# Kernel tuning notes

Measured on AMD Instinct MI355X. Metric: run time of the kernel, lower is better.

The kernel has to match this reference:

```python
import jax, jax.numpy as jnp
import numpy as np

N = 8192
D = 512
H = 256
K_TOPK = 21  # k + 1 with k = 20
EPS_NORM = 1e-12
EPS_DEG = 1e-10


def setup_inputs() -> dict:
    key = jax.random.key(0)
    ks = jax.random.split(key, 10)
    s = 0.02  # small init scale so similarities are well-behaved
    return {
        "features": jax.random.normal(ks[0], (N, D), jnp.float32),
        "masked_features": jax.random.normal(ks[1], (N, D), jnp.float32),
        "W1": jax.random.normal(ks[2], (D, D), jnp.float32) * s,
        "b1": jax.random.normal(ks[3], (D,), jnp.float32) * s,
        "W2": jax.random.normal(ks[4], (D, D), jnp.float32) * s,
        "b2": jax.random.normal(ks[5], (D,), jnp.float32) * s,
        "Wg1": jax.random.normal(ks[6], (D, H), jnp.float32) * s,
        "bg1": jax.random.normal(ks[7], (H,), jnp.float32) * s,
        "Wg2": jax.random.normal(ks[8], (H, D), jnp.float32) * s,
        "bg2": jax.random.normal(ks[9], (D,), jnp.float32) * s,
    }


def reference(features, masked_features, W1, b1, W2, b2, Wg1, bg1, Wg2, bg2):
    # ---- graph generator MLP ----
    h = jax.nn.relu(features @ W1 + b1)            # [N, D]
    emb = h @ W2 + b2                              # [N, D]
    norm = jnp.linalg.norm(emb, axis=1, keepdims=True)
    emb = emb / jnp.maximum(norm, EPS_NORM)        # F.normalize(dim=1, p=2)
    sim = emb @ emb.T                              # [N, N] cosine similarity

    # ---- top-k mask (k+1 neighbors), zero diagonal ----
    _, idx = jax.lax.top_k(sim, K_TOPK)            # [N, K]
    rows = jnp.arange(N)[:, None]
    mask = jnp.zeros((N, N), sim.dtype).at[rows, idx].set(1.0)
    mask = mask * (1.0 - jnp.eye(N, dtype=sim.dtype))  # fill_diagonal_(0)
    mask = jax.lax.stop_gradient(mask)
    sim = jax.nn.relu(sim * mask)

    # ---- symmetrize ----
    gen_adj = (sim + sim.T) * 0.5                  # [N, N]

    # ---- degree norm: D^{-1/2} (A + I) D^{-1/2} ----
    A = gen_adj + jnp.eye(N, dtype=gen_adj.dtype)
    inv_sqrt_deg = 1.0 / (jnp.sqrt(A.sum(axis=1)) + EPS_DEG)
    A = inv_sqrt_deg[:, None] * A * inv_sqrt_deg[None, :]

    # ---- two dense GCN hops (dropout inert in eval mode) ----
    h1 = jax.nn.relu(A @ (masked_features @ Wg1 + bg1))  # [N, H]
    h3 = A @ (h1 @ Wg2 + bg2)                            # [N, D]
    return h3, gen_adj
```

## Files before the change

### kernel.cpp

```cpp
#include <hip/hip_runtime.h>
#include <cstdint>
#include <cstddef>

#define NN 8192
#define DD 512
#define HH 256
#define KTOP 21
#define CCAP 192
#define CMIN 48
#define ECAP 224
#define NBIN 1024

typedef __attribute__((ext_vector_type(8))) __bf16 bf16x8;
typedef __attribute__((ext_vector_type(4))) float f32x4;

__device__ __forceinline__ unsigned short f2bf(float x) {
    unsigned u = __float_as_uint(x);
    u += 0x7fffu + ((u >> 16) & 1u);
    return (unsigned short)(u >> 16);
}
__device__ __forceinline__ float bf2f(unsigned short h) {
    return __uint_as_float(((unsigned)h) << 16);
}
__device__ __forceinline__ unsigned ordkey(float x) {
    unsigned b = __float_as_uint(x);
    return b ^ (((int)b >> 31) | 0x80000000u);
}

#define GLD16(gp, lp) __builtin_amdgcn_global_load_lds( \
    (const __attribute__((address_space(1))) unsigned int*)(gp), \
    (__attribute__((address_space(3))) unsigned int*)(lp), 16, 0, 0)

template<bool TRANSB, int ACT>
__global__ __launch_bounds__(256)
void sgemm128(const float* __restrict__ A, const float* __restrict__ B,
              const float* __restrict__ bias, float* __restrict__ C,
              int M, int N, int K) {
    constexpr int BM = 128, BN = 128, BK = 16;
    __shared__ float As[BK][BM + 4];
    __shared__ float Bs[BK][BN + 4];

    const int tiles_n = N / BN;
    const int by = blockIdx.x / tiles_n;
    const int bx = blockIdx.x % tiles_n;
    const int row0 = by * BM, col0 = bx * BN;
    const int tid = threadIdx.x;
    const int tx = tid & 15, ty = tid >> 4;

    float acc[8][8];
#pragma unroll
    for (int m = 0; m < 8; ++m)
#pragma unroll
        for (int n = 0; n < 8; ++n) acc[m][n] = 0.f;

    for (int k0 = 0; k0 < K; k0 += BK) {
#pragma unroll
        for (int l = 0; l < 2; ++l) {
            int f = tid + l * 256;
            int r = f >> 2, c4 = f & 3;
            float4 v = *reinterpret_cast<const float4*>(
                A + (size_t)(row0 + r) * K + k0 + c4 * 4);
            As[c4 * 4 + 0][r] = v.x;
            As[c4 * 4 + 1][r] = v.y;
            As[c4 * 4 + 2][r] = v.z;
            As[c4 * 4 + 3][r] = v.w;
        }
        if (TRANSB) {
#pragma unroll
            for (int l = 0; l < 2; ++l) {
                int f = tid + l * 256;
                int r = f >> 2, c4 = f & 3;
                float4 v = *reinterpret_cast<const float4*>(
                    B + (size_t)(col0 + r) * K + k0 + c4 * 4);
                Bs[c4 * 4 + 0][r] = v.x;
                Bs[c4 * 4 + 1][r] = v.y;
                Bs[c4 * 4 + 2][r] = v.z;
                Bs[c4 * 4 + 3][r] = v.w;
            }
        } else {
#pragma unroll
            for (int l = 0; l < 2; ++l) {
                int f = tid + l * 256;
                int kr = f >> 5, n4 = f & 31;
                *reinterpret_cast<float4*>(&Bs[kr][n4 * 4]) =
                    *reinterpret_cast<const float4*>(
                        B + (size_t)(k0 + kr) * N + col0 + n4 * 4);
            }
        }
        __syncthreads();

#pragma unroll
        for (int kk = 0; kk < BK; ++kk) {
            float a[8], b[8];
            *(float4*)&a[0] = *(const float4*)&As[kk][ty * 8];
            *(float4*)&a[4] = *(const float4*)&As[kk][ty * 8 + 4];
            *(float4*)&b[0] = *(const float4*)&Bs[kk][tx * 8];
            *(float4*)&b[4] = *(const float4*)&Bs[kk][tx * 8 + 4];
#pragma unroll
            for (int m = 0; m < 8; ++m)
#pragma unroll
                for (int n = 0; n < 8; ++n)
                    acc[m][n] = fmaf(a[m], b[n], acc[m][n]);
        }
        __syncthreads();
    }

    const int crow = row0 + ty * 8;
    const int ccol = col0 + tx * 8;
    float bv[8];
#pragma unroll
    for (int n = 0; n < 8; ++n) bv[n] = bias ? bias[ccol + n] : 0.f;
#pragma unroll
    for (int m = 0; m < 8; ++m) {
        float o[8];
#pragma unroll
        for (int n = 0; n < 8; ++n) {
            float t = acc[m][n] + bv[n];
            if (ACT == 1) t = fmaxf(t, 0.f);
            o[n] = t;
        }
        *reinterpret_cast<float4*>(C + (size_t)(crow + m) * N + ccol)     = *(float4*)&o[0];
        *reinterpret_cast<float4*>(C + (size_t)(crow + m) * N + ccol + 4) = *(float4*)&o[4];
    }
}

__global__ __launch_bounds__(256)
void rownorm_kernel(float* __restrict__ emb) {
    const int row = blockIdx.x, tid = threadIdx.x;
    float* rp = emb + (size_t)row * DD;
    float v0 = rp[tid], v1 = rp[tid + 256];
    float sum = v0 * v0 + v1 * v1;
#pragma unroll
    for (int off = 32; off > 0; off >>= 1) sum += __shfl_down(sum, off, 64);
    __shared__ float ws[4];
    __shared__ float sc_sh;
    if ((tid & 63) == 0) ws[tid >> 6] = sum;
    __syncthreads();
    if (tid == 0) {
        float n = sqrtf(ws[0] + ws[1] + ws[2] + ws[3]);
        sc_sh = 1.0f / fmaxf(n, 1e-12f);
    }
    __syncthreads();
    float sc = sc_sh;
    rp[tid] = v0 * sc;
    rp[tid + 256] = v1 * sc;
}

__global__ __launch_bounds__(256)
void cast_bf16_kernel(const float* __restrict__ e, unsigned short* __restrict__ hi) {
    const int i = (blockIdx.x * 256 + threadIdx.x) * 4;
    float4 v = *reinterpret_cast<const float4*>(e + i);
    ushort4 h;
    h.x = f2bf(v.x); h.y = f2bf(v.y); h.z = f2bf(v.z); h.w = f2bf(v.w);
    *reinterpret_cast<ushort4*>(hi + i) = h;
}

__global__ __launch_bounds__(256)
void simgemm_bf16(const unsigned short* __restrict__ Ehi,
                  unsigned short* __restrict__ Cb) {
    const int bid = blockIdx.x;
    const int swz = (bid & 7) * 512 + (bid >> 3);
    const int by = swz >> 6, bx = swz & 63;

    __shared__ unsigned short Ah[128 * 32];
    __shared__ unsigned short Bh[128 * 32];

    const int tid = threadIdx.x, lane = tid & 63, wid = tid >> 6;
    const int wm = wid >> 1, wn = wid & 1;
    const int fr = lane & 15, fq = lane >> 4;
    const int lrow = lane >> 2;
    const int lcol8 = (lane & 3) * 8;

    const size_t arow0 = (size_t)by * 128;
    const size_t brow0 = (size_t)bx * 128;

    f32x4 acc[4][4];
#pragma unroll
    for (int m = 0; m < 4; ++m)
#pragma unroll
        for (int n = 0; n < 4; ++n) acc[m][n] = (f32x4){0.f, 0.f, 0.f, 0.f};

    for (int k0 = 0; k0 < DD; k0 += 32) {
#pragma unroll
        for (int i = 0; i < 2; ++i) {
            const int chunk = wid + i * 4;
            const int grow = chunk * 16 + lrow;
            GLD16(Ehi + (arow0 + grow) * DD + (k0 + lcol8), Ah + chunk * 512);
            GLD16(Ehi + (brow0 + grow) * DD + (k0 + lcol8), Bh + chunk * 512);
        }
        __syncthreads();

        bf16x8 ah[4], bh[4];
#pragma unroll
        for (int mf = 0; mf < 4; ++mf)
            ah[mf] = *(const bf16x8*)&Ah[(wm * 64 + mf * 16 + fr) * 32 + fq * 8];
#pragma unroll
        for (int nf = 0; nf < 4; ++nf)
            bh[nf] = *(const bf16x8*)&Bh[(wn * 64 + nf * 16 + fr) * 32 + fq * 8];
#pragma unroll
        for (int mf = 0; mf < 4; ++mf)
#pragma unroll
            for (int nf = 0; nf < 4; ++nf)
                acc[mf][nf] = __builtin_amdgcn_mfma_f32_16x16x32_bf16(ah[mf], bh[nf], acc[mf][nf], 0, 0, 0);
        __syncthreads();
    }

#pragma unroll
    for (int mf = 0; mf < 4; ++mf) {
#pragma unroll
        for (int nf = 0; nf < 4; ++nf) {
            const size_t row = arow0 + wm * 64 + mf * 16 + fq * 4;
            const int col = bx * 128 + wn * 64 + nf * 16 + fr;
#pragma unroll
            for (int r2 = 0; r2 < 4; ++r2)
                Cb[(row + r2) * NN + col] = f2bf(acc[mf][nf][r2]);
        }
    }
}

__global__ __launch_bounds__(256)
void topk_cand_kernel(const unsigned short* __restrict__ simb,
                      int* __restrict__ cand, int* __restrict__ ccnt) {
    const int row = blockIdx.x;
    const int tid = threadIdx.x;
    const int lane = tid & 63, wave = tid >> 6;
    const uint4* rp = reinterpret_cast<const uint4*>(simb + (size_t)row * NN);

    uint4 q[4];
#pragma unroll
    for (int t = 0; t < 4; ++t) q[t] = rp[t * 256 + tid];
    unsigned pk[16];
#pragma unroll
    for (int t = 0; t < 4; ++t) {
        pk[t * 4 + 0] = q[t].x; pk[t * 4 + 1] = q[t].y;
        pk[t * 4 + 2] = q[t].z; pk[t * 4 + 3] = q[t].w;
    }

    __shared__ int hist[NBIN];
    for (int b = tid; b < NBIN; b += 256) hist[b] = 0;
    __syncthreads();

    short bins[32];
#pragma unroll
    for (int u = 0; u < 16; ++u) {
        float flo = __uint_as_float(pk[u] << 16);
        float fhi = __uint_as_float(pk[u] & 0xFFFF0000u);
        int blo = (int)(flo * (float)NBIN); blo = max(0, min(NBIN - 1, blo));
        int bhi = (int)(fhi * (float)NBIN); bhi = max(0, min(NBIN - 1, bhi));
        bins[u * 2]     = (short)blo;
        bins[u * 2 + 1] = (short)bhi;
        atomicAdd(&hist[blo], 1);
        atomicAdd(&hist[bhi], 1);
    }
    __syncthreads();

    __shared__ int s_bstar;
    if (wave == 0) {
        int cum = 0, found = -1;
        for (int c0 = NBIN - 1; c0 >= 0 && found < 0; c0 -= 64) {
            int b = c0 - lane;
            int cnt = (b >= 0) ? hist[b] : 0;
            int sc = cnt;
#pragma unroll
            for (int off = 1; off < 64; off <<= 1) {
                int o = __shfl_up(sc, off, 64);
                if (lane >= off) sc += o;
            }
            int chunk_total = __shfl(sc, 63, 64);
            bool hit = (cum + sc >= CMIN);
            unsigned long long mh = __ballot(hit);
            if (mh) found = c0 - (__ffsll((long long)mh) - 1);
            else cum += chunk_total;
        }
        if (found < 0) found = 0;
        if (lane == 0) s_bstar = found;
    }
    __syncthreads();
    const int bstar = s_bstar;

    int cnt = 0;
#pragma unroll
    for (int i = 0; i < 32; ++i) cnt += (bins[i] >= bstar) ? 1 : 0;
    int sc = cnt;
#pragma unroll
    for (int off = 1; off < 64; off <<= 1) {
        int o = __shfl_up(sc, off, 64);
        if (lane >= off) sc += o;
    }
    __shared__ int wtot[4];
    if (lane == 63) wtot[wave] = sc;
    __syncthreads();
    int base = sc - cnt;
#pragma unroll
    for (int w = 0; w < 4; ++w)
        if (w < wave) base += wtot[w];
    int total = wtot[0] + wtot[1] + wtot[2] + wtot[3];

    int pos = base;
#pragma unroll
    for (int u = 0; u < 16; ++u) {
#pragma unroll
        for (int h = 0; h < 2; ++h) {
            if (bins[u * 2 + h] >= bstar) {
                if (pos < CCAP) {
                    int col = ((u >> 2) * 256 + tid) * 8 + (u & 3) * 2 + h;
                    cand[(size_t)row * CCAP + pos] = col;
                }
                pos++;
            }
        }
    }
    if (tid == 0) ccnt[row] = min(total, CCAP);
}

__global__ __launch_bounds__(256)
void refine_kernel(const float* __restrict__ emb, const int* __restrict__ cand,
                   const int* __restrict__ ccnt,
                   int* __restrict__ tidx, float* __restrict__ tval) {
    const int row = blockIdx.x;
    const int tid = threadIdx.x, lane = tid & 63, wv = tid >> 6;
    const int cnt = ccnt[row];
    __shared__ float sval[CCAP];
    __shared__ int   sidx[CCAP];
    const float* ei = emb + (size_t)row * DD;

    float4 a0 = reinterpret_cast<const float4*>(ei)[lane * 2];
    float4 a1 = reinterpret_cast<const float4*>(ei)[lane * 2 + 1];

    for (int base = wv * 2; base < cnt; base += 8) {
#pragma unroll
        for (int q = 0; q < 2; ++q) {
            int c = base + q;
            if (c >= cnt) break;
            const int j = cand[(size_t)row * CCAP + c];
            const float* ej = emb + (size_t)j * DD;
            float4 b0 = reinterpret_cast<const float4*>(ej)[lane * 2];
            float4 b1 = reinterpret_cast<const float4*>(ej)[lane * 2 + 1];
            float s = 0.f;
            s = fmaf(a0.x, b0.x, s); s = fmaf(a0.y, b0.y, s);
            s = fmaf(a0.z, b0.z, s); s = fmaf(a0.w, b0.w, s);
            s = fmaf(a1.x, b1.x, s); s = fmaf(a1.y, b1.y, s);
            s = fmaf(a1.z, b1.z, s); s = fmaf(a1.w, b1.w, s);
#pragma unroll
            for (int off = 32; off > 0; off >>= 1) s += __shfl_xor(s, off, 64);
            if (lane == 0) { sval[c] = s; sidx[c] = j; }
        }
    }
    __syncthreads();

    if (wv == 0) {
        float v[3]; int id[3];
#pragma unroll
        for (int k = 0; k < 3; ++k) {
            int s = lane + 64 * k;
            if (s < cnt) { v[k] = sval[s]; id[k] = sidx[s]; }
            else         { v[k] = -INFINITY; id[k] = 0x7fffffff; }
        }
#pragma unroll 1
        for (int sel = 0; sel < KTOP; ++sel) {
            float bv = v[0]; int bi = id[0];
#pragma unroll
            for (int k = 1; k < 3; ++k)
                if (v[k] > bv || (v[k] == bv && id[k] < bi)) { bv = v[k]; bi = id[k]; }
#pragma unroll
            for (int off = 1; off < 64; off <<= 1) {
                float ov = __shfl_xor(bv, off, 64);
                int   oi = __shfl_xor(bi, off, 64);
                if (ov > bv || (ov == bv && oi < bi)) { bv = ov; bi = oi; }
            }
            if (lane == 0) {
                tval[(size_t)row * KTOP + sel] = bv;
                tidx[(size_t)row * KTOP + sel] = bi;
            }
#pragma unroll
            for (int k = 0; k < 3; ++k)
                if (id[k] == bi) { v[k] = -INFINITY; id[k] = 0x7fffffff; }
        }
    }
}

__global__ __launch_bounds__(256)
void scatter_kernel(const int* __restrict__ tidx, const float* __restrict__ tval,
                    float* __restrict__ adj, int* __restrict__ ecnt,
                    int* __restrict__ ej, float* __restrict__ ev) {
    int t = blockIdx.x * 256 + threadIdx.x;
    if (t >= NN * KTOP) return;
    int i = t / KTOP;
    int j = tidx[t];
    if (j == i || j < 0) return;
    float v = tval[t];
    if (v <= 0.f) return;
    v *= 0.5f;
    atomicAdd(adj + (size_t)i * NN + j, v);
    atomicAdd(adj + (size_t)j * NN + i, v);
    int pi = atomicAdd(ecnt + i, 1);
    if (pi < ECAP) { ej[(size_t)i * ECAP + pi] = j; ev[(size_t)i * ECAP + pi] = v; }
    int pj = atomicAdd(ecnt + j, 1);
    if (pj < ECAP) { ej[(size_t)j * ECAP + pj] = i; ev[(size_t)j * ECAP + pj] = v; }
}

__global__ __launch_bounds__(256)
void sortdeg_kernel(int* __restrict__ ej, float* __restrict__ ev,
                    const int* __restrict__ ecnt, const float* __restrict__ adj,
                    float* __restrict__ sdeg) {
    const int row = blockIdx.x, tid = threadIdx.x;
    const int lane = tid & 63, wave = tid >> 6;
    const int nraw = ecnt[row];
    __shared__ float ws[4];

    if (nraw > ECAP) {
        const float4* rp = reinterpret_cast<const float4*>(adj + (size_t)row * NN);
        float sum = 0.f;
        for (int f = tid; f < NN / 4; f += 256) {
            float4 v = rp[f];
            sum += (v.x + v.y) + (v.z + v.w);
        }
#pragma unroll
        for (int off = 32; off > 0; off >>= 1) sum += __shfl_down(sum, off, 64);
        if (lane == 0) ws[wave] = sum;
        __syncthreads();
        if (tid == 0)
            sdeg[row] = 1.0f / (sqrtf(1.0f + ws[0] + ws[1] + ws[2] + ws[3]) + 1e-10f);
        return;
    }

    const int n = nraw;
    __shared__ int   lj[ECAP];
    __shared__ float lv[ECAP];
    __shared__ unsigned long long skey[ECAP];
    __shared__ int   oj[ECAP];
    __shared__ float ov[ECAP];
    if (tid < n) {
        int  jv = ej[(size_t)row * ECAP + tid];
        float vv = ev[(size_t)row * ECAP + tid];
        lj[tid] = jv; lv[tid] = vv;
        skey[tid] = ((unsigned long long)(unsigned)jv << 32) | (unsigned long long)ordkey(vv);
    }
    __syncthreads();
    if (tid < n) {
        unsigned long long mk = skey[tid];
        int rank = 0;
        for (int u = 0; u < n; ++u) {
            unsigned long long ku = skey[u];
            rank += (ku < mk || (ku == mk && u < tid)) ? 1 : 0;
        }
        oj[rank] = lj[tid];
        ov[rank] = lv[tid];
    }
    __syncthreads();
    if (tid < n) {
        ej[(size_t)row * ECAP + tid] = oj[tid];
        ev[(size_t)row * ECAP + tid] = ov[tid];
    }
    if (tid == 0) {
        float deg = 1.0f;
        for (int e = 0; e < n; ++e) deg += ov[e];
        sdeg[row] = 1.0f / (sqrtf(deg) + 1e-10f);
    }
}

template<int COLS, bool DORELU>
__global__ __launch_bounds__(256)
void spmm_edges(const int* __restrict__ ej, const float* __restrict__ ev,
                const int* __restrict__ ecnt, const float* __restrict__ adj,
                const float* __restrict__ sdeg,
                const float* __restrict__ X, float* __restrict__ Y) {
    constexpr int CPT = COLS / 256;
    const int i = blockIdx.x;
    const int tid = threadIdx.x;
    const int lane = tid & 63, wave = tid >> 6;
    const float si = sdeg[i];
    const int nraw = ecnt[i];

    float acc[CPT];
#pragma unroll
    for (int c = 0; c < CPT; ++c) acc[c] = 0.f;

    if (nraw <= ECAP) {
        __shared__ int   s_j[ECAP];
        __shared__ float s_w[ECAP];
        if (tid < nraw) {
            int j = ej[(size_t)i * ECAP + tid];
            s_j[tid] = j;
            s_w[tid] = ev[(size_t)i * ECAP + tid] * sdeg[j];
        }
        __syncthreads();
#pragma unroll 4
        for (int e = 0; e < nraw; ++e) {
            int j = s_j[e];
            float we = s_w[e];
#pragma unroll
            for (int c = 0; c < CPT; ++c)
                acc[c] += we * X[(size_t)j * COLS + tid + c * 256];
        }
    } else {
        __shared__ int   s_j[256];
        __shared__ float s_w[256];
        __shared__ int   s_cnt[4];
        const float* rowp = adj + (size_t)i * NN;
        for (int j0 = 0; j0 < NN; j0 += 256) {
            float w = rowp[j0 + tid];
            bool nz = (w != 0.f);
            unsigned long long m = __ballot(nz);
            unsigned long long ltmask = (lane == 0) ? 0ull : (~0ull >> (64 - lane));
            int pre = __popcll(m & ltmask);
            if (lane == 0) s_cnt[wave] = __popcll(m);
            __syncthreads();
            int base = 0;
#pragma unroll
            for (int q = 0; q < 4; ++q)
                if (q < wave) base += s_cnt[q];
            int total = s_cnt[0] + s_cnt[1] + s_cnt[2] + s_cnt[3];
            if (nz) {
                int p = base + pre;
                s_j[p] = j0 + tid;
                s_w[p] = w * sdeg[j0 + tid];
            }
            __syncthreads();
            for (int e = 0; e < total; ++e) {
                int j = s_j[e];
                float we = s_w[e];
#pragma unroll
                for (int c = 0; c < CPT; ++c)
                    acc[c] += we * X[(size_t)j * COLS + tid + c * 256];
            }
            __syncthreads();
        }
    }

#pragma unroll
    for (int c = 0; c < CPT; ++c) {
        float val = si * (acc[c] + si * X[(size_t)i * COLS + tid + c * 256]);
        if (DORELU) val = fmaxf(val, 0.f);
        Y[(size_t)i * COLS + tid + c * 256] = val;
    }
}

extern "C" void kernel_launch(void* const* d_in, const int* in_sizes, int n_in,
                              void* d_out, int out_size, void* d_ws, size_t ws_size,
                              hipStream_t stream) {
    const float* features = (const float*)d_in[0];
    const float* masked   = (const float*)d_in[1];
    const float* W1  = (const float*)d_in[2];
    const float* b1  = (const float*)d_in[3];
    const float* W2  = (const float*)d_in[4];
    const float* b2  = (const float*)d_in[5];
    const float* Wg1 = (const float*)d_in[6];
    const float* bg1 = (const float*)d_in[7];
    const float* Wg2 = (const float*)d_in[8];
    const float* bg2 = (const float*)d_in[9];

    float* out_h3  = (float*)d_out;
    float* out_adj = (float*)d_out + (size_t)NN * DD;
    unsigned short* simb = (unsigned short*)out_adj;

    float* h    = (float*)d_ws;
    unsigned short* hi = (unsigned short*)h;
    float* emb  = h + (size_t)NN * DD;
    float* tail = emb + (size_t)NN * DD;
    float* tval = tail;
    int*   tidx = (int*)(tval + (size_t)NN * KTOP);
    float* sdeg = (float*)(tidx + (size_t)NN * KTOP);
    int*   ecnt = (int*)(sdeg + NN);
    int*   ccnt = ecnt + NN;
    int*   elj  = ccnt + NN;
    float* elv  = (float*)(elj + (size_t)NN * ECAP);
    int*   cand = (int*)h;
    float* x1 = emb;
    float* h1 = emb + (size_t)NN * HH;
    float* x2 = h;

    dim3 blk(256);

    sgemm128<false, 1><<<dim3((NN / 128) * (DD / 128)), blk, 0, stream>>>(
        features, W1, b1, h, NN, DD, DD);
    sgemm128<false, 0><<<dim3((NN / 128) * (DD / 128)), blk, 0, stream>>>(
        h, W2, b2, emb, NN, DD, DD);
    rownorm_kernel<<<dim3(NN), blk, 0, stream>>>(emb);
    cast_bf16_kernel<<<dim3(NN * DD / 1024), blk, 0, stream>>>(emb, hi);
    simgemm_bf16<<<dim3(4096), blk, 0, stream>>>(hi, simb);
    topk_cand_kernel<<<dim3(NN), blk, 0, stream>>>(simb, cand, ccnt);
    refine_kernel<<<dim3(NN), blk, 0, stream>>>(emb, cand, ccnt, tidx, tval);
    hipMemsetAsync(out_adj, 0, (size_t)NN * NN * sizeof(float), stream);
    hipMemsetAsync(ecnt, 0, (size_t)NN * sizeof(int), stream);
    scatter_kernel<<<dim3((NN * KTOP + 255) / 256), blk, 0, stream>>>(
        tidx, tval, out_adj, ecnt, elj, elv);
    sortdeg_kernel<<<dim3(NN), blk, 0, stream>>>(elj, elv, ecnt, out_adj, sdeg);
    sgemm128<false, 0><<<dim3((NN / 128) * (HH / 128)), blk, 0, stream>>>(
        masked, Wg1, bg1, x1, NN, HH, DD);
    spmm_edges<HH, true><<<dim3(NN), blk, 0, stream>>>(
        elj, elv, ecnt, out_adj, sdeg, x1, h1);
    sgemm128<false, 0><<<dim3((NN / 128) * (DD / 128)), blk, 0, stream>>>(
        h1, Wg2, bg2, x2, NN, DD, HH);
    spmm_edges<DD, false><<<dim3(NN), blk, 0, stream>>>(
        elj, elv, ecnt, out_adj, sdeg, x2, out_h3);
}
```

Before: 802.1 us.

## Use split-bf16 MFMA for GCN GEMMs, fuse rownorm cast, custom zero kernel

The two GCN projection GEMMs move from the fp32 SIMT sgemm to a bf16x3 split-precision MFMA kernel (hi*hi + hi*lo + lo*hi). This needs extra split and weight-transpose kernels. The bf16 cast of the normalized embeddings is folded into the row-normalization kernel, which removes one pass over the embedding. The two memsets are replaced by a single grid-stride zero kernel. The aim is to trade fp32 FMA throughput for matrix-core throughput at slightly lower precision, at the cost of several extra small launches and workspace traffic.

After: 754.8 us. 5.9% less time.

```diff
diff --git a/kernel.cpp b/kernel.cpp
--- a/kernel.cpp
+++ b/kernel.cpp
@@ -125,7 +125,7 @@
 }
 
 __global__ __launch_bounds__(256)
-void rownorm_kernel(float* __restrict__ emb) {
+void rownorm_emit_kernel(float* __restrict__ emb, unsigned short* __restrict__ ehi) {
     const int row = blockIdx.x, tid = threadIdx.x;
     float* rp = emb + (size_t)row * DD;
     float v0 = rp[tid], v1 = rp[tid + 256];
@@ -142,17 +142,47 @@
     }
     __syncthreads();
     float sc = sc_sh;
-    rp[tid] = v0 * sc;
-    rp[tid + 256] = v1 * sc;
-}
-
-__global__ __launch_bounds__(256)
-void cast_bf16_kernel(const float* __restrict__ e, unsigned short* __restrict__ hi) {
+    v0 *= sc; v1 *= sc;
+    rp[tid] = v0;
+    rp[tid + 256] = v1;
+    ehi[(size_t)row * DD + tid]       = f2bf(v0);
+    ehi[(size_t)row * DD + tid + 256] = f2bf(v1);
+}
+
+__global__ __launch_bounds__(256)
+void split_kernel(const float* __restrict__ e, unsigned short* __restrict__ hi,
+                  unsigned short* __restrict__ lo) {
     const int i = (blockIdx.x * 256 + threadIdx.x) * 4;
     float4 v = *reinterpret_cast<const float4*>(e + i);
-    ushort4 h;
-    h.x = f2bf(v.x); h.y = f2bf(v.y); h.z = f2bf(v.z); h.w = f2bf(v.w);
+    ushort4 h, l;
+    h.x = f2bf(v.x); l.x = f2bf(v.x - bf2f(h.x));
+    h.y = f2bf(v.y); l.y = f2bf(v.y - bf2f(h.y));
+    h.z = f2bf(v.z); l.z = f2bf(v.z - bf2f(h.z));
+    h.w = f2bf(v.w); l.w = f2bf(v.w - bf2f(h.w));
     *reinterpret_cast<ushort4*>(hi + i) = h;
+    *reinterpret_cast<ushort4*>(lo + i) = l;
+}
+
+__global__ __launch_bounds__(256)
+void wtrans_kernel(const float* __restrict__ W, unsigned short* __restrict__ Thi,
+                   unsigned short* __restrict__ Tlo, int K, int N) {
+    int t = blockIdx.x * 256 + threadIdx.x;
+    if (t >= K * N) return;
+    int k = t / N, n = t - k * N;
+    float x = W[t];
+    unsigned short h = f2bf(x);
+    Thi[(size_t)n * K + k] = h;
+    Tlo[(size_t)n * K + k] = f2bf(x - bf2f(h));
+}
+
+__global__ __launch_bounds__(256)
+void zero_kernel(float4* __restrict__ adj4, float4* __restrict__ ecnt4) {
+    const float4 z = {0.f, 0.f, 0.f, 0.f};
+    size_t gid = (size_t)blockIdx.x * 256 + threadIdx.x;
+    const size_t stride = (size_t)gridDim.x * 256;
+    const size_t total = (size_t)NN * NN / 4;
+    for (size_t i = gid; i < total; i += stride) adj4[i] = z;
+    if (gid < NN / 4) ecnt4[gid] = z;
 }
 
 __global__ __launch_bounds__(256)
@@ -214,6 +244,86 @@
 #pragma unroll
             for (int r2 = 0; r2 < 4; ++r2)
                 Cb[(row + r2) * NN + col] = f2bf(acc[mf][nf][r2]);
+        }
+    }
+}
+
+template<int KDIM>
+__global__ __launch_bounds__(256)
+void mfma_nt_bias(const unsigned short* __restrict__ Ahi,
+                  const unsigned short* __restrict__ Alo,
+                  const unsigned short* __restrict__ Bhi,
+                  const unsigned short* __restrict__ Blo,
+                  const float* __restrict__ bias, float* __restrict__ C, int N) {
+    const int tiles_n = N / 128;
+    const int by = blockIdx.x / tiles_n, bx = blockIdx.x % tiles_n;
+
+    __shared__ unsigned short Ah[128 * 32];
+    __shared__ unsigned short Al[128 * 32];
+    __shared__ unsigned short Bh[128 * 32];
+    __shared__ unsigned short Bl[128 * 32];
+
+    const int tid = threadIdx.x, lane = tid & 63, wid = tid >> 6;
+    const int wm = wid >> 1, wn = wid & 1;
+    const int fr = lane & 15, fq = lane >> 4;
+    const int lrow = lane >> 2;
+    const int lcol8 = (lane & 3) * 8;
+
+    const size_t arow0 = (size_t)by * 128;
+    const size_t brow0 = (size_t)bx * 128;
+
+    f32x4 acc[4][4];
+#pragma unroll
+    for (int m = 0; m < 4; ++m)
+#pragma unroll
+        for (int n = 0; n < 4; ++n) acc[m][n] = (f32x4){0.f, 0.f, 0.f, 0.f};
+
+    for (int k0 = 0; k0 < KDIM; k0 += 32) {
+#pragma unroll
+        for (int i = 0; i < 2; ++i) {
+            const int chunk = wid + i * 4;
+            const int grow = chunk * 16 + lrow;
+            GLD16(Ahi + (arow0 + grow) * KDIM + (k0 + lcol8), Ah + chunk * 512);
+            GLD16(Alo + (arow0 + grow) * KDIM + (k0 + lcol8), Al + chunk * 512);
+            GLD16(Bhi + (brow0 + grow) * KDIM + (k0 + lcol8), Bh + chunk * 512);
+            GLD16(Blo + (brow0 + grow) * KDIM + (k0 + lcol8), Bl + chunk * 512);
+        }
+        __syncthreads();
+
+        bf16x8 ah[4], al[4], bh[4], bl[4];
+#pragma unroll
+        for (int mf = 0; mf < 4; ++mf) {
+            const int r = wm * 64 + mf * 16 + fr;
+            ah[mf] = *(const bf16x8*)&Ah[r * 32 + fq * 8];
+            al[mf] = *(const bf16x8*)&Al[r * 32 + fq * 8];
+        }
+#pragma unroll
+        for (int nf = 0; nf < 4; ++nf) {
+            const int r = wn * 64 + nf * 16 + fr;
+            bh[nf] = *(const bf16x8*)&Bh[r * 32 + fq * 8];
+            bl[nf] = *(const bf16x8*)&Bl[r * 32 + fq * 8];
+        }
+#pragma unroll
+        for (int mf = 0; mf < 4; ++mf)
+#pragma unroll
+            for (int nf = 0; nf < 4; ++nf) {
+                acc[mf][nf] = __builtin_amdgcn_mfma_f32_16x16x32_bf16(ah[mf], bh[nf], acc[mf][nf], 0, 0, 0);
+                acc[mf][nf] = __builtin_amdgcn_mfma_f32_16x16x32_bf16(ah[mf], bl[nf], acc[mf][nf], 0, 0, 0);
+                acc[mf][nf] = __builtin_amdgcn_mfma_f32_16x16x32_bf16(al[mf], bh[nf], acc[mf][nf], 0, 0, 0);
+            }
+        __syncthreads();
+    }
+
+#pragma unroll
+    for (int mf = 0; mf < 4; ++mf) {
+#pragma unroll
+        for (int nf = 0; nf < 4; ++nf) {
+            const size_t row = arow0 + wm * 64 + mf * 16 + fq * 4;
+            const int col = bx * 128 + wn * 64 + nf * 16 + fr;
+            const float bv = bias[col];
+#pragma unroll
+            for (int r2 = 0; r2 < 4; ++r2)
+                C[(row + r2) * N + col] = acc[mf][nf][r2] + bv;
         }
     }
 }
@@ -554,10 +664,23 @@
     float* out_adj = (float*)d_out + (size_t)NN * DD;
     unsigned short* simb = (unsigned short*)out_adj;
 
-    float* h    = (float*)d_ws;
-    unsigned short* hi = (unsigned short*)h;
-    float* emb  = h + (size_t)NN * DD;
-    float* tail = emb + (size_t)NN * DD;
+    float* Areg = (float*)d_ws;
+    float* Breg = Areg + (size_t)NN * DD;
+    float* tail = Breg + (size_t)NN * DD;
+
+    float* h    = Areg;
+    unsigned short* ehi = (unsigned short*)Areg;
+    int*   cand = (int*)(Areg + (size_t)NN * DD / 2);
+    unsigned short* mhi = (unsigned short*)Areg;
+    unsigned short* mlo = mhi + (size_t)NN * DD;
+    unsigned short* h1hi = (unsigned short*)Areg;
+    unsigned short* h1lo = h1hi + (size_t)NN * HH;
+
+    float* emb = Breg;
+    float* x1  = Breg;
+    float* h1  = Breg + (size_t)NN * HH;
+    float* x2  = Breg;
+
     float* tval = tail;
     int*   tidx = (int*)(tval + (size_t)NN * KTOP);
     float* sdeg = (float*)(tidx + (size_t)NN * KTOP);
@@ -565,10 +688,10 @@
     int*   ccnt = ecnt + NN;
     int*   elj  = ccnt + NN;
     float* elv  = (float*)(elj + (size_t)NN * ECAP);
-    int*   cand = (int*)h;
-    float* x1 = emb;
-    float* h1 = emb + (size_t)NN * HH;
-    float* x2 = h;
+    unsigned short* wt1hi = (unsigned short*)(elv + (size_t)NN * ECAP);
+    unsigned short* wt1lo = wt1hi + (size_t)HH * DD;
+    unsigned short* wt2hi = wt1lo + (size_t)HH * DD;
+    unsigned short* wt2lo = wt2hi + (size_t)DD * HH;
 
     dim3 blk(256);
 
@@ -576,22 +699,25 @@
         features, W1, b1, h, NN, DD, DD);
     sgemm128<false, 0><<<dim3((NN / 128) * (DD / 128)), blk, 0, stream>>>(
         h, W2, b2, emb, NN, DD, DD);
-    rownorm_kernel<<<dim3(NN), blk, 0, stream>>>(emb);
-    cast_bf16_kernel<<<dim3(NN * DD / 1024), blk, 0, stream>>>(emb, hi);
-    simgemm_bf16<<<dim3(4096), blk, 0, stream>>>(hi, simb);
+    rownorm_emit_kernel<<<dim3(NN), blk, 0, stream>>>(emb, ehi);
+    simgemm_bf16<<<dim3(4096), blk, 0, stream>>>(ehi, simb);
     topk_cand_kernel<<<dim3(NN), blk, 0, stream>>>(simb, cand, ccnt);
     refine_kernel<<<dim3(NN), blk, 0, stream>>>(emb, cand, ccnt, tidx, tval);
-    hipMemsetAsync(out_adj, 0, (size_t)NN * NN * sizeof(float), stream);
-    hipMemsetAsync(ecnt, 0, (size_t)NN * sizeof(int), stream);
+    zero_kernel<<<dim3(2048), blk, 0, stream>>>(
+        (float4*)out_adj, (float4*)ecnt);
     scatter_kernel<<<dim3((NN * KTOP + 255) / 256), blk, 0, stream>>>(
         tidx, tval, out_adj, ecnt, elj, elv);
     sortdeg_kernel<<<dim3(NN), blk, 0, stream>>>(elj, elv, ecnt, out_adj, sdeg);
-    sgemm128<false, 0><<<dim3((NN / 128) * (HH / 128)), blk, 0, stream>>>(
-        masked, Wg1, bg1, x1, NN, HH, DD);
+    split_kernel<<<dim3(NN * DD / 1024), blk, 0, stream>>>(masked, mhi, mlo);
+    wtrans_kernel<<<dim3(DD * HH / 256), blk, 0, stream>>>(Wg1, wt1hi, wt1lo, DD, HH);
+    mfma_nt_bias<DD><<<dim3((NN / 128) * (HH / 128)), blk, 0, stream>>>(
+        mhi, mlo, wt1hi, wt1lo, bg1, x1, HH);
     spmm_edges<HH, true><<<dim3(NN), blk, 0, stream>>>(
         elj, elv, ecnt, out_adj, sdeg, x1, h1);
-    sgemm128<false, 0><<<dim3((NN / 128) * (DD / 128)), blk, 0, stream>>>(
-        h1, Wg2, bg2, x2, NN, DD, HH);
+    split_kernel<<<dim3(NN * HH / 1024), blk, 0, stream>>>(h1, h1hi, h1lo);
+    wtrans_kernel<<<dim3(HH * DD / 256), blk, 0, stream>>>(Wg2, wt2hi, wt2lo, HH, DD);
+    mfma_nt_bias<HH><<<dim3((NN / 128) * (DD / 128)), blk, 0, stream>>>(
+        h1hi, h1lo, wt2hi, wt2lo, bg2, x2, DD);
     spmm_edges<DD, false><<<dim3(NN), blk, 0, stream>>>(
         elj, elv, ecnt, out_adj, sdeg, x2, out_h3);
 }
```
